# Optimization experiments

Measured on AMD Instinct MI355X. Metric: run time of the kernel, lower is better.

The kernel has to match this reference:

```python
import jax, jax.numpy as jnp
import numpy as np

N_NODES = 100000
N_EDGES = 1600000
D = 128
BN_EPS = 1e-5
GINE_EPS = 0.0  # GINEConv default eps=0, train_eps=False


def setup_inputs() -> dict:
    key = jax.random.key(0)
    ks = jax.random.split(key, 9)
    x = jax.random.normal(ks[0], (N_NODES, D), dtype=jnp.float32)
    edge_index = jax.random.randint(ks[1], (2, N_EDGES), 0, N_NODES, dtype=jnp.int64)
    edge_attr = jax.random.normal(ks[2], (N_EDGES, D), dtype=jnp.float32)
    s = 1.0 / np.sqrt(D)
    W1 = jax.random.uniform(ks[3], (D, D), jnp.float32, -s, s)
    b1 = jax.random.uniform(ks[4], (D,), jnp.float32, -s, s)
    W2 = jax.random.uniform(ks[5], (D, D), jnp.float32, -s, s)
    b2 = jax.random.uniform(ks[6], (D,), jnp.float32, -s, s)
    gamma = jnp.ones((D,), jnp.float32)
    beta = jnp.zeros((D,), jnp.float32)
    return {"x": x, "edge_index": edge_index, "edge_attr": edge_attr,
            "W1": W1, "b1": b1, "W2": W2, "b2": b2,
            "gamma": gamma, "beta": beta}


def reference(x, edge_index, edge_attr, W1, b1, W2, b2, gamma, beta):
    src, dst = edge_index[0], edge_index[1]
    # per-edge message: ReLU(x_j + e_ij)
    msg = jax.nn.relu(x[src] + edge_attr)                      # [E, D]
    # sum aggregation to target nodes
    agg = jax.ops.segment_sum(msg, dst, num_segments=x.shape[0])  # [N, D]
    h = (1.0 + GINE_EPS) * x + agg
    # MLP: Linear -> ReLU -> Linear
    h = jax.nn.relu(h @ W1 + b1) @ W2 + b2
    # BatchNorm1d (training mode: batch stats, biased variance)
    mean = jnp.mean(h, axis=0)
    var = jnp.var(h, axis=0)
    h = (h - mean) * jax.lax.rsqrt(var + BN_EPS) * gamma + beta
    return jax.nn.relu(h)
```

## Files before the change

kernel.cpp:

```cpp
#include <hip/hip_runtime.h>

#define BN_EPS 1e-5f

typedef __bf16 bf16;
typedef __bf16 bf16x8 __attribute__((ext_vector_type(8)));
typedef __bf16 bf16x4 __attribute__((ext_vector_type(4)));
typedef float f32x4 __attribute__((ext_vector_type(4)));

__global__ void prep_kernel(const int* __restrict__ ei, int* __restrict__ deg, int E,
                            const float4* __restrict__ x4, bf16x4* __restrict__ xb4, int n4) {
    const int half = 2048 * 256;
    if (blockIdx.x < 2048) {
        int i = blockIdx.x * blockDim.x + threadIdx.x;
        for (; i < E; i += half) atomicAdd(&deg[ei[E + i]], 1);
    } else {
        int i = (blockIdx.x - 2048) * blockDim.x + threadIdx.x;
        for (; i < n4; i += half) {
            const float4 v = x4[i];
            bf16x4 o;
            o[0] = (bf16)v.x; o[1] = (bf16)v.y; o[2] = (bf16)v.z; o[3] = (bf16)v.w;
            xb4[i] = o;
        }
    }
}

__global__ void wprep_kernel(const float* __restrict__ W1, const float* __restrict__ W2,
                             bf16* __restrict__ Wt1, bf16* __restrict__ Wt2) {
    const int c = blockIdx.x;
    const int k = threadIdx.x;
    Wt1[c * 128 + k] = (bf16)W1[k * 128 + c];
    Wt2[c * 128 + k] = (bf16)W2[k * 128 + c];
}

__global__ void scanA(const int* __restrict__ deg, int* __restrict__ rowStart,
                      int* __restrict__ blockSums, int N) {
    __shared__ int sd[256];
    const int t = threadIdx.x;
    const int idx = blockIdx.x * 1024 + t * 4;
    int d0 = 0, d1 = 0, d2 = 0, d3 = 0;
    if (idx + 3 < N) { int4 v = *(const int4*)&deg[idx]; d0 = v.x; d1 = v.y; d2 = v.z; d3 = v.w; }
    else {
        if (idx     < N) d0 = deg[idx];
        if (idx + 1 < N) d1 = deg[idx + 1];
        if (idx + 2 < N) d2 = deg[idx + 2];
    }
    const int s = d0 + d1 + d2 + d3;
    sd[t] = s;
    __syncthreads();
    #pragma unroll
    for (int off = 1; off < 256; off <<= 1) {
        const int v = (t >= off) ? sd[t - off] : 0;
        __syncthreads();
        sd[t] += v;
        __syncthreads();
    }
    const int ex = sd[t] - s;
    if (idx     < N) rowStart[idx]     = ex;
    if (idx + 1 < N) rowStart[idx + 1] = ex + d0;
    if (idx + 2 < N) rowStart[idx + 2] = ex + d0 + d1;
    if (idx + 3 < N) rowStart[idx + 3] = ex + d0 + d1 + d2;
    if (t == 255) blockSums[blockIdx.x] = sd[255];
}

__global__ void scanB(int* __restrict__ blockSums, int nblk) {
    __shared__ int sd[256];
    const int t = threadIdx.x;
    const int s = (t < nblk) ? blockSums[t] : 0;
    sd[t] = s;
    __syncthreads();
    #pragma unroll
    for (int off = 1; off < 256; off <<= 1) {
        const int v = (t >= off) ? sd[t - off] : 0;
        __syncthreads();
        sd[t] += v;
        __syncthreads();
    }
    if (t < nblk) blockSums[t] = sd[t] - s;
}

__global__ void scanC(int* __restrict__ rowStart, int* __restrict__ cursor,
                      const int* __restrict__ blockSums, int N) {
    int i = blockIdx.x * blockDim.x + threadIdx.x;
    const int stride = gridDim.x * blockDim.x;
    for (; i < N; i += stride) {
        const int v = rowStart[i] + blockSums[i >> 10];
        rowStart[i] = v;
        cursor[i]   = v;
    }
}

__global__ void scatter_kernel(const int* __restrict__ ei, int* __restrict__ cursor,
                               int2* __restrict__ sPair, int E) {
    int i = blockIdx.x * blockDim.x + threadIdx.x;
    const int stride = gridDim.x * blockDim.x;
    for (; i < E; i += stride) {
        const int dst = ei[E + i];
        const int src = ei[i];
        const int pos = atomicAdd(&cursor[dst], 1);
        sPair[pos] = make_int2(i, src);
    }
}

__launch_bounds__(256)
__global__ void agg_kernel(const float* __restrict__ x, const bf16* __restrict__ xb,
                           const float* __restrict__ ea, const int2* __restrict__ sPair,
                           const int* __restrict__ rowStart, const int* __restrict__ deg,
                           bf16* __restrict__ h0b, int N) {
    const int wid = (blockIdx.x * blockDim.x + threadIdx.x) >> 6;
    if (wid >= N) return;
    const int lane = threadIdx.x & 63;
    const int half = lane >> 5;
    const int c    = lane & 31;

    const int rs = rowStart[wid];
    const int dg = deg[wid];

    f32x4 acc = {0.f, 0.f, 0.f, 0.f};

    int done = 0;
    while (done < dg) {
        const int batch = (dg - done < 64) ? (dg - done) : 64;
        int2 p = make_int2(0, 0);
        if (lane < batch) p = sPair[rs + done + lane];
        int i = 0;
        for (; i + 8 <= batch; i += 8) {
            int e[4], s[4];
            #pragma unroll
            for (int q = 0; q < 4; q++) {
                e[q] = __shfl(p.x, i + 2 * q + half);
                s[q] = __shfl(p.y, i + 2 * q + half);
            }
            f32x4 a[4]; bf16x4 xr[4];
            #pragma unroll
            for (int q = 0; q < 4; q++) {
                a[q]  = __builtin_nontemporal_load((const f32x4*)ea + (((size_t)e[q]) << 5) + c);
                xr[q] = *((const bf16x4*)xb + (((size_t)s[q]) << 5) + c);
            }
            #pragma unroll
            for (int q = 0; q < 4; q++) {
                acc[0] += fmaxf(a[q][0] + (float)xr[q][0], 0.f);
                acc[1] += fmaxf(a[q][1] + (float)xr[q][1], 0.f);
                acc[2] += fmaxf(a[q][2] + (float)xr[q][2], 0.f);
                acc[3] += fmaxf(a[q][3] + (float)xr[q][3], 0.f);
            }
        }
        if (i + 4 <= batch) {
            const int eA = __shfl(p.x, i + half);
            const int sA = __shfl(p.y, i + half);
            const int eB = __shfl(p.x, i + 2 + half);
            const int sB = __shfl(p.y, i + 2 + half);
            const f32x4 a0 = __builtin_nontemporal_load((const f32x4*)ea + (((size_t)eA) << 5) + c);
            const bf16x4 x0 = *((const bf16x4*)xb + (((size_t)sA) << 5) + c);
            const f32x4 a1 = __builtin_nontemporal_load((const f32x4*)ea + (((size_t)eB) << 5) + c);
            const bf16x4 x1 = *((const bf16x4*)xb + (((size_t)sB) << 5) + c);
            acc[0] += fmaxf(a0[0] + (float)x0[0], 0.f) + fmaxf(a1[0] + (float)x1[0], 0.f);
            acc[1] += fmaxf(a0[1] + (float)x0[1], 0.f) + fmaxf(a1[1] + (float)x1[1], 0.f);
            acc[2] += fmaxf(a0[2] + (float)x0[2], 0.f) + fmaxf(a1[2] + (float)x1[2], 0.f);
            acc[3] += fmaxf(a0[3] + (float)x0[3], 0.f) + fmaxf(a1[3] + (float)x1[3], 0.f);
            i += 4;
        }
        if (i + 2 <= batch) {
            const int eA = __shfl(p.x, i + half);
            const int sA = __shfl(p.y, i + half);
            const f32x4 a0 = __builtin_nontemporal_load((const f32x4*)ea + (((size_t)eA) << 5) + c);
            const bf16x4 x0 = *((const bf16x4*)xb + (((size_t)sA) << 5) + c);
            acc[0] += fmaxf(a0[0] + (float)x0[0], 0.f);
            acc[1] += fmaxf(a0[1] + (float)x0[1], 0.f);
            acc[2] += fmaxf(a0[2] + (float)x0[2], 0.f);
            acc[3] += fmaxf(a0[3] + (float)x0[3], 0.f);
            i += 2;
        }
        if (i < batch) {
            const int eA = __shfl(p.x, i);
            const int sA = __shfl(p.y, i);
            if (half == 0) {
                const f32x4 a0 = __builtin_nontemporal_load((const f32x4*)ea + (((size_t)eA) << 5) + c);
                const bf16x4 x0 = *((const bf16x4*)xb + (((size_t)sA) << 5) + c);
                acc[0] += fmaxf(a0[0] + (float)x0[0], 0.f);
                acc[1] += fmaxf(a0[1] + (float)x0[1], 0.f);
                acc[2] += fmaxf(a0[2] + (float)x0[2], 0.f);
                acc[3] += fmaxf(a0[3] + (float)x0[3], 0.f);
            }
        }
        done += batch;
    }

    acc[0] += __shfl_xor(acc[0], 32);
    acc[1] += __shfl_xor(acc[1], 32);
    acc[2] += __shfl_xor(acc[2], 32);
    acc[3] += __shfl_xor(acc[3], 32);

    if (half == 0) {
        const f32x4 xv = *((const f32x4*)x + (((size_t)wid) << 5) + c);
        bf16x4 o;
        o[0] = (bf16)(acc[0] + xv[0]);
        o[1] = (bf16)(acc[1] + xv[1]);
        o[2] = (bf16)(acc[2] + xv[2]);
        o[3] = (bf16)(acc[3] + xv[3]);
        *((bf16x4*)h0b + (((size_t)wid) << 5) + c) = o;
    }
}

__launch_bounds__(256)
__global__ void mlp_kernel(const bf16* __restrict__ h0b,
                           const bf16* __restrict__ Wt1, const float* __restrict__ b1,
                           const bf16* __restrict__ Wt2, const float* __restrict__ b2,
                           float* __restrict__ out, double* __restrict__ stats, int N) {
    __shared__ bf16 Xs[128][136];
    __shared__ float SredS[4][128];
    __shared__ float SredQ[4][128];
    const int tid  = threadIdx.x;
    const int lane = tid & 63;
    const int wv   = tid >> 6;
    const int base = blockIdx.x * 128;

    {
        const int r  = tid >> 1;
        const int c0 = (tid & 1) * 64;
        const int n  = base + r;
        bf16x8* dst = (bf16x8*)&Xs[r][c0];
        if (n < N) {
            const bf16x8* src = (const bf16x8*)(h0b + (size_t)n * 128 + c0);
            #pragma unroll
            for (int q = 0; q < 8; q++) dst[q] = src[q];
        } else {
            bf16x8 z;
            #pragma unroll
            for (int k = 0; k < 8; k++) z[k] = (bf16)0.f;
            #pragma unroll
            for (int q = 0; q < 8; q++) dst[q] = z;
        }
    }

    const int colq = lane & 15;
    const int kq   = lane >> 4;
    f32x4 accm[2][8];
    #pragma unroll
    for (int tr = 0; tr < 2; tr++)
        #pragma unroll
        for (int tc = 0; tc < 8; tc++) accm[tr][tc] = (f32x4){0.f, 0.f, 0.f, 0.f};

    #pragma unroll
    for (int ks = 0; ks < 4; ks++) {
        const int ko = 32 * ks + kq * 8;
        const bf16x8 a0 = *(const bf16x8*)&Xs[32 * wv + colq][ko];
        const bf16x8 a1 = *(const bf16x8*)&Xs[32 * wv + 16 + colq][ko];
        #pragma unroll
        for (int tc = 0; tc < 8; tc++) {
            const bf16x8 bf = *(const bf16x8*)&Wt1[(size_t)(16 * tc + colq) * 128 + ko];
            accm[0][tc] = __builtin_amdgcn_mfma_f32_16x16x32_bf16(a0, bf, accm[0][tc], 0, 0, 0);
            accm[1][tc] = __builtin_amdgcn_mfma_f32_16x16x32_bf16(a1, bf, accm[1][tc], 0, 0, 0);
        }
    }

    #pragma unroll
    for (int tc = 0; tc < 8; tc++) {
        const float bj = b1[16 * tc + colq];
        #pragma unroll
        for (int tr = 0; tr < 2; tr++) {
            #pragma unroll
            for (int r = 0; r < 4; r++) {
                const int row = 32 * wv + 16 * tr + 4 * kq + r;
                Xs[row][16 * tc + colq] = (bf16)fmaxf(accm[tr][tc][r] + bj, 0.f);
            }
        }
    }

    #pragma unroll
    for (int tr = 0; tr < 2; tr++)
        #pragma unroll
        for (int tc = 0; tc < 8; tc++) accm[tr][tc] = (f32x4){0.f, 0.f, 0.f, 0.f};

    #pragma unroll
    for (int ks = 0; ks < 4; ks++) {
        const int ko = 32 * ks + kq * 8;
        const bf16x8 a0 = *(const bf16x8*)&Xs[32 * wv + colq][ko];
        const bf16x8 a1 = *(const bf16x8*)&Xs[32 * wv + 16 + colq][ko];
        #pragma unroll
        for (int tc = 0; tc < 8; tc++) {
            const bf16x8 bf = *(const bf16x8*)&Wt2[(size_t)(16 * tc + colq) * 128 + ko];
            accm[0][tc] = __builtin_amdgcn_mfma_f32_16x16x32_bf16(a0, bf, accm[0][tc], 0, 0, 0);
            accm[1][tc] = __builtin_amdgcn_mfma_f32_16x16x32_bf16(a1, bf, accm[1][tc], 0, 0, 0);
        }
    }

    #pragma unroll
    for (int tc = 0; tc < 8; tc++) {
        const int col = 16 * tc + colq;
        const float bj = b2[col];
        float sv = 0.f, qv = 0.f;
        #pragma unroll
        for (int tr = 0; tr < 2; tr++) {
            #pragma unroll
            for (int r = 0; r < 4; r++) {
                const int n = base + 32 * wv + 16 * tr + 4 * kq + r;
                if (n < N) {
                    const float h2 = accm[tr][tc][r] + bj;
                    out[(size_t)n * 128 + col] = h2;
                    sv += h2; qv += h2 * h2;
                }
            }
        }
        sv += __shfl_xor(sv, 16); qv += __shfl_xor(qv, 16);
        sv += __shfl_xor(sv, 32); qv += __shfl_xor(qv, 32);
        if (kq == 0) {
            SredS[wv][col] = sv;
            SredQ[wv][col] = qv;
        }
    }

    __syncthreads();
    if (tid < 128) {
        const float ss = SredS[0][tid] + SredS[1][tid] + SredS[2][tid] + SredS[3][tid];
        const float qq = SredQ[0][tid] + SredQ[1][tid] + SredQ[2][tid] + SredQ[3][tid];
        unsafeAtomicAdd(&stats[tid],       (double)ss);
        unsafeAtomicAdd(&stats[128 + tid], (double)qq);
    }
}

__global__ void bn_kernel(float4* __restrict__ out4, const double* __restrict__ stats,
                          const float* __restrict__ gamma, const float* __restrict__ beta,
                          float invN, int n4) {
    __shared__ float s_sc[128];
    __shared__ float s_bs[128];
    const int tid = threadIdx.x;
    if (tid < 128) {
        const float mean = (float)(stats[tid] * (double)invN);
        const float ex2  = (float)(stats[128 + tid] * (double)invN);
        const float var  = ex2 - mean * mean;
        const float rstd = rsqrtf(var + BN_EPS);
        const float sc = rstd * gamma[tid];
        s_sc[tid] = sc;
        s_bs[tid] = beta[tid] - mean * sc;
    }
    __syncthreads();
    int i = blockIdx.x * blockDim.x + tid;
    const int stride = gridDim.x * blockDim.x;
    for (; i < n4; i += stride) {
        const int c4 = (i & 31) << 2;
        float4 v = out4[i];
        const float4 sc = *(const float4*)&s_sc[c4];
        const float4 bs = *(const float4*)&s_bs[c4];
        v.x = fmaxf(fmaf(v.x, sc.x, bs.x), 0.f);
        v.y = fmaxf(fmaf(v.y, sc.y, bs.y), 0.f);
        v.z = fmaxf(fmaf(v.z, sc.z, bs.z), 0.f);
        v.w = fmaxf(fmaf(v.w, sc.w, bs.w), 0.f);
        out4[i] = v;
    }
}

extern "C" void kernel_launch(void* const* d_in, const int* in_sizes, int n_in,
                              void* d_out, int out_size, void* d_ws, size_t ws_size,
                              hipStream_t stream) {
    const float* x     = (const float*)d_in[0];
    const int*   ei    = (const int*)d_in[1];
    const float* ea    = (const float*)d_in[2];
    const float* W1    = (const float*)d_in[3];
    const float* b1    = (const float*)d_in[4];
    const float* W2    = (const float*)d_in[5];
    const float* b2    = (const float*)d_in[6];
    const float* gamma = (const float*)d_in[7];
    const float* beta  = (const float*)d_in[8];
    float* out = (float*)d_out;

    const int N = in_sizes[0] / 128;
    const int E = in_sizes[1] / 2;

    char* w = (char*)d_ws;
    size_t o = 0;
    int* deg = (int*)(w + o);         o += ((size_t)N * 4 + 15) & ~(size_t)15;
    const size_t zeroLen = o + 2048;
    double* stats = (double*)(w + o); o += 2048;
    int* rowStart = (int*)(w + o);    o += ((size_t)N * 4 + 15) & ~(size_t)15;
    int* cursor   = (int*)(w + o);    o += ((size_t)N * 4 + 15) & ~(size_t)15;
    int* blockSums= (int*)(w + o);    o += 1024;
    int2* sPair   = (int2*)(w + o);   o += (size_t)E * 8;
    bf16* Wt1     = (bf16*)(w + o);   o += 32768;
    bf16* Wt2     = (bf16*)(w + o);   o += 32768;
    bf16* xb      = (bf16*)(w + o);   o += (size_t)N * 128 * 2;
    bf16* h0b     = (bf16*)(w + o);   o += (size_t)N * 128 * 2;

    hipMemsetAsync(d_ws, 0, zeroLen, stream);

    prep_kernel<<<4096, 256, 0, stream>>>(ei, deg, E, (const float4*)x, (bf16x4*)xb, N * 32);
    wprep_kernel<<<128, 128, 0, stream>>>(W1, W2, Wt1, Wt2);

    const int nblk = (N + 1023) / 1024;
    scanA<<<nblk, 256, 0, stream>>>(deg, rowStart, blockSums, N);
    scanB<<<1, 256, 0, stream>>>(blockSums, nblk);
    scanC<<<256, 256, 0, stream>>>(rowStart, cursor, blockSums, N);
    scatter_kernel<<<2048, 256, 0, stream>>>(ei, cursor, sPair, E);

    agg_kernel<<<(N * 64 + 255) / 256, 256, 0, stream>>>(x, xb, ea, sPair, rowStart, deg, h0b, N);

    mlp_kernel<<<(N + 127) / 128, 256, 0, stream>>>(h0b, Wt1, b1, Wt2, b2, out, stats, N);

    bn_kernel<<<2048, 256, 0, stream>>>((float4*)out, stats, gamma, beta, 1.0f / (float)N, N * 32);
}
```

Before: 498.6 us.

## Fuse setup, scan and scatter stages into one cooperative kernel with grid syncs

```diff
diff --git a/kernel.cpp b/kernel.cpp
--- a/kernel.cpp
+++ b/kernel.cpp
@@ -1,4 +1,7 @@
 #include <hip/hip_runtime.h>
+#include <hip/hip_cooperative_groups.h>
+
+namespace cg = cooperative_groups;
 
 #define BN_EPS 1e-5f
 
@@ -7,93 +10,85 @@
 typedef __bf16 bf16x4 __attribute__((ext_vector_type(4)));
 typedef float f32x4 __attribute__((ext_vector_type(4)));
 
-__global__ void prep_kernel(const int* __restrict__ ei, int* __restrict__ deg, int E,
-                            const float4* __restrict__ x4, bf16x4* __restrict__ xb4, int n4) {
-    const int half = 2048 * 256;
-    if (blockIdx.x < 2048) {
-        int i = blockIdx.x * blockDim.x + threadIdx.x;
-        for (; i < E; i += half) atomicAdd(&deg[ei[E + i]], 1);
-    } else {
-        int i = (blockIdx.x - 2048) * blockDim.x + threadIdx.x;
-        for (; i < n4; i += half) {
-            const float4 v = x4[i];
-            bf16x4 o;
-            o[0] = (bf16)v.x; o[1] = (bf16)v.y; o[2] = (bf16)v.z; o[3] = (bf16)v.w;
-            xb4[i] = o;
-        }
-    }
-}
-
-__global__ void wprep_kernel(const float* __restrict__ W1, const float* __restrict__ W2,
-                             bf16* __restrict__ Wt1, bf16* __restrict__ Wt2) {
-    const int c = blockIdx.x;
-    const int k = threadIdx.x;
-    Wt1[c * 128 + k] = (bf16)W1[k * 128 + c];
-    Wt2[c * 128 + k] = (bf16)W2[k * 128 + c];
-}
-
-__global__ void scanA(const int* __restrict__ deg, int* __restrict__ rowStart,
-                      int* __restrict__ blockSums, int N) {
+__launch_bounds__(256)
+__global__ void setup_kernel(const int* __restrict__ ei, int E,
+                             const f32x4* __restrict__ x4, bf16x4* __restrict__ xb4, int n4,
+                             const float* __restrict__ W1, const float* __restrict__ W2,
+                             bf16* __restrict__ Wt1, bf16* __restrict__ Wt2,
+                             int* __restrict__ deg, int* __restrict__ rowStart,
+                             int* __restrict__ cursor, int* __restrict__ blockSums,
+                             double* __restrict__ stats, int2* __restrict__ sPair, int N) {
+    cg::grid_group grid = cg::this_grid();
     __shared__ int sd[256];
-    const int t = threadIdx.x;
-    const int idx = blockIdx.x * 1024 + t * 4;
-    int d0 = 0, d1 = 0, d2 = 0, d3 = 0;
-    if (idx + 3 < N) { int4 v = *(const int4*)&deg[idx]; d0 = v.x; d1 = v.y; d2 = v.z; d3 = v.w; }
-    else {
-        if (idx     < N) d0 = deg[idx];
-        if (idx + 1 < N) d1 = deg[idx + 1];
-        if (idx + 2 < N) d2 = deg[idx + 2];
-    }
-    const int s = d0 + d1 + d2 + d3;
-    sd[t] = s;
-    __syncthreads();
-    #pragma unroll
-    for (int off = 1; off < 256; off <<= 1) {
-        const int v = (t >= off) ? sd[t - off] : 0;
+    const int tid  = threadIdx.x;
+    const int gtid = blockIdx.x * 256 + tid;
+    const int gsz  = gridDim.x * 256;
+
+    for (int i = gtid; i < N; i += gsz) deg[i] = 0;
+    if (gtid < 256) stats[gtid] = 0.0;
+    grid.sync();
+
+    for (int i = gtid; i < E; i += gsz) atomicAdd(&deg[ei[E + i]], 1);
+    for (int i = gtid; i < n4; i += gsz) {
+        const f32x4 v = x4[i];
+        bf16x4 o;
+        o[0] = (bf16)v[0]; o[1] = (bf16)v[1]; o[2] = (bf16)v[2]; o[3] = (bf16)v[3];
+        xb4[i] = o;
+    }
+    if (gtid < 16384) {
+        const int c = gtid >> 7, k = gtid & 127;
+        Wt1[c * 128 + k] = (bf16)W1[k * 128 + c];
+        Wt2[c * 128 + k] = (bf16)W2[k * 128 + c];
+    }
+    grid.sync();
+
+    const int nchunk = (N + 255) >> 8;
+    for (int chunk = blockIdx.x; chunk < nchunk; chunk += gridDim.x) {
+        const int idx = (chunk << 8) + tid;
+        const int d = (idx < N) ? deg[idx] : 0;
+        sd[tid] = d;
         __syncthreads();
-        sd[t] += v;
+        #pragma unroll
+        for (int off = 1; off < 256; off <<= 1) {
+            const int v = (tid >= off) ? sd[tid - off] : 0;
+            __syncthreads();
+            sd[tid] += v;
+            __syncthreads();
+        }
+        if (idx < N) rowStart[idx] = sd[tid] - d;
+        if (tid == 255) blockSums[chunk] = sd[255];
         __syncthreads();
     }
-    const int ex = sd[t] - s;
-    if (idx     < N) rowStart[idx]     = ex;
-    if (idx + 1 < N) rowStart[idx + 1] = ex + d0;
-    if (idx + 2 < N) rowStart[idx + 2] = ex + d0 + d1;
-    if (idx + 3 < N) rowStart[idx + 3] = ex + d0 + d1 + d2;
-    if (t == 255) blockSums[blockIdx.x] = sd[255];
-}
-
-__global__ void scanB(int* __restrict__ blockSums, int nblk) {
-    __shared__ int sd[256];
-    const int t = threadIdx.x;
-    const int s = (t < nblk) ? blockSums[t] : 0;
-    sd[t] = s;
-    __syncthreads();
-    #pragma unroll
-    for (int off = 1; off < 256; off <<= 1) {
-        const int v = (t >= off) ? sd[t - off] : 0;
+    grid.sync();
+
+    if (blockIdx.x == 0) {
+        const int j0 = 2 * tid, j1 = 2 * tid + 1;
+        const int e0 = (j0 < nchunk) ? blockSums[j0] : 0;
+        const int e1 = (j1 < nchunk) ? blockSums[j1] : 0;
+        const int s = e0 + e1;
+        sd[tid] = s;
         __syncthreads();
-        sd[t] += v;
-        __syncthreads();
-    }
-    if (t < nblk) blockSums[t] = sd[t] - s;
-}
-
-__global__ void scanC(int* __restrict__ rowStart, int* __restrict__ cursor,
-                      const int* __restrict__ blockSums, int N) {
-    int i = blockIdx.x * blockDim.x + threadIdx.x;
-    const int stride = gridDim.x * blockDim.x;
-    for (; i < N; i += stride) {
-        const int v = rowStart[i] + blockSums[i >> 10];
+        #pragma unroll
+        for (int off = 1; off < 256; off <<= 1) {
+            const int v = (tid >= off) ? sd[tid - off] : 0;
+            __syncthreads();
+            sd[tid] += v;
+            __syncthreads();
+        }
+        const int ex = sd[tid] - s;
+        if (j0 < nchunk) blockSums[j0] = ex;
+        if (j1 < nchunk) blockSums[j1] = ex + e0;
+    }
+    grid.sync();
+
+    for (int i = gtid; i < N; i += gsz) {
+        const int v = rowStart[i] + blockSums[i >> 8];
         rowStart[i] = v;
         cursor[i]   = v;
     }
-}
-
-__global__ void scatter_kernel(const int* __restrict__ ei, int* __restrict__ cursor,
-                               int2* __restrict__ sPair, int E) {
-    int i = blockIdx.x * blockDim.x + threadIdx.x;
-    const int stride = gridDim.x * blockDim.x;
-    for (; i < E; i += stride) {
+    grid.sync();
+
+    for (int i = gtid; i < E; i += gsz) {
         const int dst = ei[E + i];
         const int src = ei[i];
         const int pos = atomicAdd(&cursor[dst], 1);
@@ -369,27 +364,26 @@
     char* w = (char*)d_ws;
     size_t o = 0;
     int* deg = (int*)(w + o);         o += ((size_t)N * 4 + 15) & ~(size_t)15;
-    const size_t zeroLen = o + 2048;
     double* stats = (double*)(w + o); o += 2048;
     int* rowStart = (int*)(w + o);    o += ((size_t)N * 4 + 15) & ~(size_t)15;
     int* cursor   = (int*)(w + o);    o += ((size_t)N * 4 + 15) & ~(size_t)15;
-    int* blockSums= (int*)(w + o);    o += 1024;
+    int* blockSums= (int*)(w + o);    o += 4096;
     int2* sPair   = (int2*)(w + o);   o += (size_t)E * 8;
     bf16* Wt1     = (bf16*)(w + o);   o += 32768;
     bf16* Wt2     = (bf16*)(w + o);   o += 32768;
     bf16* xb      = (bf16*)(w + o);   o += (size_t)N * 128 * 2;
     bf16* h0b     = (bf16*)(w + o);   o += (size_t)N * 128 * 2;
 
-    hipMemsetAsync(d_ws, 0, zeroLen, stream);
-
-    prep_kernel<<<4096, 256, 0, stream>>>(ei, deg, E, (const float4*)x, (bf16x4*)xb, N * 32);
-    wprep_kernel<<<128, 128, 0, stream>>>(W1, W2, Wt1, Wt2);
-
-    const int nblk = (N + 1023) / 1024;
-    scanA<<<nblk, 256, 0, stream>>>(deg, rowStart, blockSums, N);
-    scanB<<<1, 256, 0, stream>>>(blockSums, nblk);
-    scanC<<<256, 256, 0, stream>>>(rowStart, cursor, blockSums, N);
-    scatter_kernel<<<2048, 256, 0, stream>>>(ei, cursor, sPair, E);
+    {
+        const int n4 = N * 32;
+        const f32x4* x4c = (const f32x4*)x;
+        bf16x4* xb4 = (bf16x4*)xb;
+        void* args[] = { (void*)&ei, (void*)&E, (void*)&x4c, (void*)&xb4, (void*)&n4,
+                         (void*)&W1, (void*)&W2, (void*)&Wt1, (void*)&Wt2,
+                         (void*)&deg, (void*)&rowStart, (void*)&cursor, (void*)&blockSums,
+                         (void*)&stats, (void*)&sPair, (void*)&N };
+        hipLaunchCooperativeKernel((void*)setup_kernel, dim3(512), dim3(256), args, 0, stream);
+    }
 
     agg_kernel<<<(N * 64 + 255) / 256, 256, 0, stream>>>(x, xb, ea, sPair, rowStart, deg, h0b, N);
 
```

Result: slower. 759.3 us (+52.3%).

## Compute edge messages in edge order and scatter fp16 rows into CSR slots

Applied to the files above, without the earlier changes.

```diff
diff --git a/kernel.cpp b/kernel.cpp
--- a/kernel.cpp
+++ b/kernel.cpp
@@ -6,9 +6,13 @@
 typedef __bf16 bf16x8 __attribute__((ext_vector_type(8)));
 typedef __bf16 bf16x4 __attribute__((ext_vector_type(4)));
 typedef float f32x4 __attribute__((ext_vector_type(4)));
+typedef _Float16 f16;
+typedef unsigned long long u64;
+
+union F16x4U { f16 h[4]; u64 u; };
 
 __global__ void prep_kernel(const int* __restrict__ ei, int* __restrict__ deg, int E,
-                            const float4* __restrict__ x4, bf16x4* __restrict__ xb4, int n4) {
+                            const f32x4* __restrict__ x4, bf16x4* __restrict__ xb4, int n4) {
     const int half = 2048 * 256;
     if (blockIdx.x < 2048) {
         int i = blockIdx.x * blockDim.x + threadIdx.x;
@@ -16,9 +20,9 @@
     } else {
         int i = (blockIdx.x - 2048) * blockDim.x + threadIdx.x;
         for (; i < n4; i += half) {
-            const float4 v = x4[i];
+            const f32x4 v = x4[i];
             bf16x4 o;
-            o[0] = (bf16)v.x; o[1] = (bf16)v.y; o[2] = (bf16)v.z; o[3] = (bf16)v.w;
+            o[0] = (bf16)v[0]; o[1] = (bf16)v[1]; o[2] = (bf16)v[2]; o[3] = (bf16)v[3];
             xb4[i] = o;
         }
     }
@@ -89,23 +93,75 @@
     }
 }
 
-__global__ void scatter_kernel(const int* __restrict__ ei, int* __restrict__ cursor,
-                               int2* __restrict__ sPair, int E) {
-    int i = blockIdx.x * blockDim.x + threadIdx.x;
-    const int stride = gridDim.x * blockDim.x;
-    for (; i < E; i += stride) {
-        const int dst = ei[E + i];
-        const int src = ei[i];
-        const int pos = atomicAdd(&cursor[dst], 1);
-        sPair[pos] = make_int2(i, src);
-    }
-}
-
 __launch_bounds__(256)
-__global__ void agg_kernel(const float* __restrict__ x, const bf16* __restrict__ xb,
-                           const float* __restrict__ ea, const int2* __restrict__ sPair,
-                           const int* __restrict__ rowStart, const int* __restrict__ deg,
-                           bf16* __restrict__ h0b, int N) {
+__global__ void msg_kernel(const int* __restrict__ ei, const bf16* __restrict__ xb,
+                           const float* __restrict__ ea, int* __restrict__ cursor,
+                           f16* __restrict__ msgS, int E) {
+    const int wvid = (blockIdx.x * blockDim.x + threadIdx.x) >> 6;
+    const int lane = threadIdx.x & 63;
+    const int half = lane >> 5;
+    const int c    = lane & 31;
+    const int base = wvid * 64;
+    if (base >= E) return;
+    const int batch = (E - base < 64) ? (E - base) : 64;
+
+    int src = 0, pos = 0;
+    if (lane < batch) {
+        src = ei[base + lane];
+        const int dst = ei[E + base + lane];
+        pos = atomicAdd(&cursor[dst], 1);
+    }
+
+    int i = 0;
+    for (; i + 4 <= batch; i += 4) {
+        const int e0 = base + i + half;
+        const int e1 = base + i + 2 + half;
+        const int s0 = __shfl(src, i + half);
+        const int s1 = __shfl(src, i + 2 + half);
+        const int p0 = __shfl(pos, i + half);
+        const int p1 = __shfl(pos, i + 2 + half);
+        const f32x4 a0 = __builtin_nontemporal_load((const f32x4*)ea + (((size_t)e0) << 5) + c);
+        const f32x4 a1 = __builtin_nontemporal_load((const f32x4*)ea + (((size_t)e1) << 5) + c);
+        const bf16x4 x0 = *((const bf16x4*)xb + (((size_t)s0) << 5) + c);
+        const bf16x4 x1 = *((const bf16x4*)xb + (((size_t)s1) << 5) + c);
+        F16x4U o0, o1;
+        #pragma unroll
+        for (int k = 0; k < 4; k++) {
+            o0.h[k] = (f16)fmaxf(a0[k] + (float)x0[k], 0.f);
+            o1.h[k] = (f16)fmaxf(a1[k] + (float)x1[k], 0.f);
+        }
+        __builtin_nontemporal_store(o0.u, (u64*)msgS + (((size_t)p0) << 5) + c);
+        __builtin_nontemporal_store(o1.u, (u64*)msgS + (((size_t)p1) << 5) + c);
+    }
+    if (i + 2 <= batch) {
+        const int e0 = base + i + half;
+        const int s0 = __shfl(src, i + half);
+        const int p0 = __shfl(pos, i + half);
+        const f32x4 a0 = __builtin_nontemporal_load((const f32x4*)ea + (((size_t)e0) << 5) + c);
+        const bf16x4 x0 = *((const bf16x4*)xb + (((size_t)s0) << 5) + c);
+        F16x4U o0;
+        #pragma unroll
+        for (int k = 0; k < 4; k++) o0.h[k] = (f16)fmaxf(a0[k] + (float)x0[k], 0.f);
+        __builtin_nontemporal_store(o0.u, (u64*)msgS + (((size_t)p0) << 5) + c);
+        i += 2;
+    }
+    if (i < batch && half == 0) {
+        const int e0 = base + i;
+        const int s0 = __shfl(src, i);
+        const int p0 = __shfl(pos, i);
+        const f32x4 a0 = __builtin_nontemporal_load((const f32x4*)ea + (((size_t)e0) << 5) + c);
+        const bf16x4 x0 = *((const bf16x4*)xb + (((size_t)s0) << 5) + c);
+        F16x4U o0;
+        #pragma unroll
+        for (int k = 0; k < 4; k++) o0.h[k] = (f16)fmaxf(a0[k] + (float)x0[k], 0.f);
+        __builtin_nontemporal_store(o0.u, (u64*)msgS + (((size_t)p0) << 5) + c);
+    }
+}
+
+__launch_bounds__(256)
+__global__ void nagg_kernel(const float* __restrict__ x, const f16* __restrict__ msgS,
+                            const int* __restrict__ rowStart, const int* __restrict__ deg,
+                            bf16* __restrict__ h0b, int N) {
     const int wid = (blockIdx.x * blockDim.x + threadIdx.x) >> 6;
     if (wid >= N) return;
     const int lane = threadIdx.x & 63;
@@ -117,72 +173,30 @@
 
     f32x4 acc = {0.f, 0.f, 0.f, 0.f};
 
-    int done = 0;
-    while (done < dg) {
-        const int batch = (dg - done < 64) ? (dg - done) : 64;
-        int2 p = make_int2(0, 0);
-        if (lane < batch) p = sPair[rs + done + lane];
-        int i = 0;
-        for (; i + 8 <= batch; i += 8) {
-            int e[4], s[4];
-            #pragma unroll
-            for (int q = 0; q < 4; q++) {
-                e[q] = __shfl(p.x, i + 2 * q + half);
-                s[q] = __shfl(p.y, i + 2 * q + half);
-            }
-            f32x4 a[4]; bf16x4 xr[4];
-            #pragma unroll
-            for (int q = 0; q < 4; q++) {
-                a[q]  = __builtin_nontemporal_load((const f32x4*)ea + (((size_t)e[q]) << 5) + c);
-                xr[q] = *((const bf16x4*)xb + (((size_t)s[q]) << 5) + c);
-            }
-            #pragma unroll
-            for (int q = 0; q < 4; q++) {
-                acc[0] += fmaxf(a[q][0] + (float)xr[q][0], 0.f);
-                acc[1] += fmaxf(a[q][1] + (float)xr[q][1], 0.f);
-                acc[2] += fmaxf(a[q][2] + (float)xr[q][2], 0.f);
-                acc[3] += fmaxf(a[q][3] + (float)xr[q][3], 0.f);
-            }
-        }
-        if (i + 4 <= batch) {
-            const int eA = __shfl(p.x, i + half);
-            const int sA = __shfl(p.y, i + half);
-            const int eB = __shfl(p.x, i + 2 + half);
-            const int sB = __shfl(p.y, i + 2 + half);
-            const f32x4 a0 = __builtin_nontemporal_load((const f32x4*)ea + (((size_t)eA) << 5) + c);
-            const bf16x4 x0 = *((const bf16x4*)xb + (((size_t)sA) << 5) + c);
-            const f32x4 a1 = __builtin_nontemporal_load((const f32x4*)ea + (((size_t)eB) << 5) + c);
-            const bf16x4 x1 = *((const bf16x4*)xb + (((size_t)sB) << 5) + c);
-            acc[0] += fmaxf(a0[0] + (float)x0[0], 0.f) + fmaxf(a1[0] + (float)x1[0], 0.f);
-            acc[1] += fmaxf(a0[1] + (float)x0[1], 0.f) + fmaxf(a1[1] + (float)x1[1], 0.f);
-            acc[2] += fmaxf(a0[2] + (float)x0[2], 0.f) + fmaxf(a1[2] + (float)x1[2], 0.f);
-            acc[3] += fmaxf(a0[3] + (float)x0[3], 0.f) + fmaxf(a1[3] + (float)x1[3], 0.f);
-            i += 4;
-        }
-        if (i + 2 <= batch) {
-            const int eA = __shfl(p.x, i + half);
-            const int sA = __shfl(p.y, i + half);
-            const f32x4 a0 = __builtin_nontemporal_load((const f32x4*)ea + (((size_t)eA) << 5) + c);
-            const bf16x4 x0 = *((const bf16x4*)xb + (((size_t)sA) << 5) + c);
-            acc[0] += fmaxf(a0[0] + (float)x0[0], 0.f);
-            acc[1] += fmaxf(a0[1] + (float)x0[1], 0.f);
-            acc[2] += fmaxf(a0[2] + (float)x0[2], 0.f);
-            acc[3] += fmaxf(a0[3] + (float)x0[3], 0.f);
-            i += 2;
-        }
-        if (i < batch) {
-            const int eA = __shfl(p.x, i);
-            const int sA = __shfl(p.y, i);
-            if (half == 0) {
-                const f32x4 a0 = __builtin_nontemporal_load((const f32x4*)ea + (((size_t)eA) << 5) + c);
-                const bf16x4 x0 = *((const bf16x4*)xb + (((size_t)sA) << 5) + c);
-                acc[0] += fmaxf(a0[0] + (float)x0[0], 0.f);
-                acc[1] += fmaxf(a0[1] + (float)x0[1], 0.f);
-                acc[2] += fmaxf(a0[2] + (float)x0[2], 0.f);
-                acc[3] += fmaxf(a0[3] + (float)x0[3], 0.f);
-            }
-        }
-        done += batch;
+    int j = 0;
+    for (; j + 4 <= dg; j += 4) {
+        const size_t r0 = (size_t)(rs + j + half) << 5;
+        const size_t r1 = (size_t)(rs + j + 2 + half) << 5;
+        F16x4U m0, m1;
+        m0.u = *((const u64*)msgS + r0 + c);
+        m1.u = *((const u64*)msgS + r1 + c);
+        #pragma unroll
+        for (int k = 0; k < 4; k++) acc[k] += (float)m0.h[k] + (float)m1.h[k];
+    }
+    if (j + 2 <= dg) {
+        const size_t r0 = (size_t)(rs + j + half) << 5;
+        F16x4U m0;
+        m0.u = *((const u64*)msgS + r0 + c);
+        #pragma unroll
+        for (int k = 0; k < 4; k++) acc[k] += (float)m0.h[k];
+        j += 2;
+    }
+    if (j < dg && half == 0) {
+        const size_t r0 = (size_t)(rs + j) << 5;
+        F16x4U m0;
+        m0.u = *((const u64*)msgS + r0 + c);
+        #pragma unroll
+        for (int k = 0; k < 4; k++) acc[k] += (float)m0.h[k];
     }
 
     acc[0] += __shfl_xor(acc[0], 32);
@@ -374,24 +388,27 @@
     int* rowStart = (int*)(w + o);    o += ((size_t)N * 4 + 15) & ~(size_t)15;
     int* cursor   = (int*)(w + o);    o += ((size_t)N * 4 + 15) & ~(size_t)15;
     int* blockSums= (int*)(w + o);    o += 1024;
-    int2* sPair   = (int2*)(w + o);   o += (size_t)E * 8;
     bf16* Wt1     = (bf16*)(w + o);   o += 32768;
     bf16* Wt2     = (bf16*)(w + o);   o += 32768;
     bf16* xb      = (bf16*)(w + o);   o += (size_t)N * 128 * 2;
     bf16* h0b     = (bf16*)(w + o);   o += (size_t)N * 128 * 2;
+    o = (o + 255) & ~(size_t)255;
+    f16* msgS     = (f16*)(w + o);    o += (size_t)E * 128 * 2;
 
     hipMemsetAsync(d_ws, 0, zeroLen, stream);
 
-    prep_kernel<<<4096, 256, 0, stream>>>(ei, deg, E, (const float4*)x, (bf16x4*)xb, N * 32);
+    prep_kernel<<<4096, 256, 0, stream>>>(ei, deg, E, (const f32x4*)x, (bf16x4*)xb, N * 32);
     wprep_kernel<<<128, 128, 0, stream>>>(W1, W2, Wt1, Wt2);
 
     const int nblk = (N + 1023) / 1024;
     scanA<<<nblk, 256, 0, stream>>>(deg, rowStart, blockSums, N);
     scanB<<<1, 256, 0, stream>>>(blockSums, nblk);
     scanC<<<256, 256, 0, stream>>>(rowStart, cursor, blockSums, N);
-    scatter_kernel<<<2048, 256, 0, stream>>>(ei, cursor, sPair, E);
-
-    agg_kernel<<<(N * 64 + 255) / 256, 256, 0, stream>>>(x, xb, ea, sPair, rowStart, deg, h0b, N);
+
+    const int nwaves_msg = (E + 63) / 64;
+    msg_kernel<<<(nwaves_msg * 64 + 255) / 256, 256, 0, stream>>>(ei, xb, ea, cursor, msgS, E);
+
+    nagg_kernel<<<(N * 64 + 255) / 256, 256, 0, stream>>>(x, msgS, rowStart, deg, h0b, N);
 
     mlp_kernel<<<(N + 127) / 128, 256, 0, stream>>>(h0b, Wt1, b1, Wt2, b2, out, stats, N);
 
```

After: 569.0 us. 1.14x slower.
